# Performance work log

Hardware: AMD Instinct MI355X
Metric: run time of the kernel (lower is better)

Reference implementation:

```python
import jax, jax.numpy as jnp
import numpy as np

B, S, I, H, O = 64, 4096, 256, 256, 128


def setup_inputs() -> dict:
    key = jax.random.key(0)
    ks = jax.random.split(key, 7)
    s_in = 1.0 / np.sqrt(I)
    s_h = 1.0 / np.sqrt(H)
    return {
        "x": jax.random.normal(ks[0], (B, S, I), dtype=jnp.float32),
        "Wax_w": jax.random.uniform(ks[1], (H, I), jnp.float32, -s_in, s_in),
        "Wax_b": jax.random.uniform(ks[2], (H,), jnp.float32, -s_in, s_in),
        "Waa_w": jax.random.uniform(ks[3], (H, H), jnp.float32, -s_h, s_h),
        "Waa_b": jax.random.uniform(ks[4], (H,), jnp.float32, -s_h, s_h),
        "Wya_w": jax.random.uniform(ks[5], (O, H), jnp.float32, -s_h, s_h),
        "Wya_b": jax.random.uniform(ks[6], (O,), jnp.float32, -s_h, s_h),
    }


def reference(x, Wax_w, Wax_b, Waa_w, Waa_b, Wya_w, Wya_b):
    # Precompute input projections for all timesteps in one big GEMM: [B,S,H]
    xp = jnp.einsum("bsi,hi->bsh", x, Wax_w) + Wax_b

    def step(a_prev, xp_t):
        a_next = jnp.tanh(xp_t + a_prev @ Waa_w.T + Waa_b)
        return a_next, None

    a0 = jnp.zeros((x.shape[0], Waa_w.shape[0]), dtype=x.dtype)
    a_last, _ = jax.lax.scan(step, a0, jnp.swapaxes(xp, 0, 1))  # scan over S
    return jax.nn.sigmoid(a_last @ Wya_w.T + Wya_b)
```

## Files before the change

### kernel.cpp

```cpp
#include <hip/hip_runtime.h>
#include <hip/hip_fp16.h>


typedef _Float16 f16x8 __attribute__((ext_vector_type(8)));
typedef _Float16 f16x4 __attribute__((ext_vector_type(4)));
typedef _Float16 f16x2 __attribute__((ext_vector_type(2)));
typedef float    f32x4 __attribute__((ext_vector_type(4)));

#define FDOT2(a, b, c) __builtin_amdgcn_fdot2((a), (b), (c), false)

template <int D>
__device__ __forceinline__ float rorf(float v) {
    return __builtin_bit_cast(float,
        __builtin_amdgcn_update_dpp(0, __builtin_bit_cast(int, v),
                                    0x120 + D, 0xF, 0xF, true));
}
template <int D>
__device__ __forceinline__ float qrot(float v) {
    constexpr int ctrl = D == 1 ? 0x93 : (D == 2 ? 0x4E : 0x39);
    return __builtin_bit_cast(float,
        __builtin_amdgcn_update_dpp(0, __builtin_bit_cast(int, v),
                                    ctrl, 0xF, 0xF, true));
}

__global__ __launch_bounds__(1024) void k_fused(
    const float* __restrict__ x, const float* __restrict__ Ww,
    const float* __restrict__ Wb, const float* __restrict__ Waa,
    const float* __restrict__ Wab, const float* __restrict__ Wya,
    const float* __restrict__ Wyb, float* __restrict__ out,
    _Float16* __restrict__ xp0, _Float16* __restrict__ xp1,
    unsigned short* __restrict__ a_state,
    int c_rnn, int c_xp, int do_rnn, int do_xp, int is_last,
    int T_C, int logT)
{
    __shared__ __align__(16) _Float16 As[128 * 264];
    __shared__ __align__(16) _Float16 aL[2][16][24];
    __shared__ float afin[256];

    const int tid  = threadIdx.x;
    const int lane = tid & 63;

    if (blockIdx.x < 64) {
        if (!do_rnn) return;
        const _Float16* xp = (c_rnn & 1) ? xp1 : xp0;
        const int w     = tid >> 6;
        const int k     = lane & 15;
        const int g     = lane >> 4;
        const int rbase = w * 16 + g * 4;
        const int myrow = rbase + (k & 3);
        const int b     = blockIdx.x;
        const bool wlane = (k & 12) == 0;

        f16x2 wr[4][8];
#pragma unroll
        for (int i = 0; i < 4; ++i) {
            const float4* wp = (const float4*)(Waa + (size_t)(rbase + ((k + i) & 3)) * 256 + k * 16);
#pragma unroll
            for (int q = 0; q < 4; ++q) {
                float4 v = wp[q];
                f16x2 t0; t0[0] = (_Float16)v.x; t0[1] = (_Float16)v.y;
                f16x2 t1; t1[0] = (_Float16)v.z; t1[1] = (_Float16)v.w;
                wr[i][2 * q]     = t0;
                wr[i][2 * q + 1] = t1;
            }
        }
        const float bias = Wab[myrow];

        if (tid < 256) {
            unsigned short v = 0;
            if (c_rnn != 0) v = a_state[b * 256 + tid];
            aL[0][tid >> 4][tid & 15] = __builtin_bit_cast(_Float16, v);
        }
        __syncthreads();

        const _Float16* xph = xp + ((size_t)(b * 256 + myrow)) * T_C;
        f16x8 xq = *(const f16x8*)(xph);
        float bx[8];
#pragma unroll
        for (int j = 0; j < 8; ++j) bx[j] = bias + (float)xq[j];

        const _Float16* rp0 = &aL[0][k][0];
        const _Float16* rp1 = &aL[1][k][0];
        _Float16* wq0 = &aL[1][w][g * 4 + k];
        _Float16* wq1 = &aL[0][w][g * 4 + k];

#define RNN_STEP(J, FIN)                                                     \
    {                                                                        \
        const _Float16* rp = ((J) & 1) ? rp1 : rp0;                          \
        uint4 r0 = *(const uint4*)(rp);                                      \
        uint4 r1 = *(const uint4*)(rp + 8);                                  \
        f16x2 a2[8];                                                         \
        a2[0] = __builtin_bit_cast(f16x2, r0.x);                             \
        a2[1] = __builtin_bit_cast(f16x2, r0.y);                             \
        a2[2] = __builtin_bit_cast(f16x2, r0.z);                             \
        a2[3] = __builtin_bit_cast(f16x2, r0.w);                             \
        a2[4] = __builtin_bit_cast(f16x2, r1.x);                             \
        a2[5] = __builtin_bit_cast(f16x2, r1.y);                             \
        a2[6] = __builtin_bit_cast(f16x2, r1.z);                             \
        a2[7] = __builtin_bit_cast(f16x2, r1.w);                             \
        float s0 = 0.f, s1 = 0.f, s2 = 0.f, s3 = 0.f;                        \
        _Pragma("unroll")                                                    \
        for (int q = 0; q < 8; ++q) {                                        \
            s0 = FDOT2(wr[0][q], a2[q], s0);                                 \
            s1 = FDOT2(wr[1][q], a2[q], s1);                                 \
            s2 = FDOT2(wr[2][q], a2[q], s2);                                 \
            s3 = FDOT2(wr[3][q], a2[q], s3);                                 \
        }                                                                    \
                 \
        float t = s0 + qrot<1>(s1);                                          \
        t += qrot<2>(s2);                                                    \
        t += qrot<3>(s3);                                                    \
        float u   = t + rorf<4>(t);                                          \
        float acc = u + rorf<8>(u);                                          \
        float z  = bx[(J)] + acc;                                            \
        float e2 = __expf(2.f * z);                                          \
        float a  = fmaf(-2.f, __builtin_amdgcn_rcpf(e2 + 1.f), 1.f);         \
        _Float16 ah = (_Float16)a;                                           \
        if (wlane) *(((J) & 1) ? wq1 : wq0) = ah;                            \
        if (FIN) {                                                           \
            afin[myrow] = a;                                                 \
            a_state[b * 256 + myrow] = __builtin_bit_cast(unsigned short, ah);\
        }                                                                    \
        asm volatile("s_waitcnt lgkmcnt(0)" ::: "memory");                   \
        __builtin_amdgcn_s_barrier();                                        \
        asm volatile("" ::: "memory");                                       \
    }

        for (int tb = 0; tb + 8 < T_C; tb += 8) {
            f16x8 xn = *(const f16x8*)(xph + tb + 8);
            RNN_STEP(0, false) RNN_STEP(1, false) RNN_STEP(2, false) RNN_STEP(3, false)
            RNN_STEP(4, false) RNN_STEP(5, false) RNN_STEP(6, false) RNN_STEP(7, false)
#pragma unroll
            for (int j = 0; j < 8; ++j) bx[j] = bias + (float)xn[j];
        }
        RNN_STEP(0, false) RNN_STEP(1, false) RNN_STEP(2, false) RNN_STEP(3, false)
        RNN_STEP(4, false) RNN_STEP(5, false) RNN_STEP(6, false) RNN_STEP(7, true)
#undef RNN_STEP

        if (is_last) {
            const int o  = tid >> 3;
            const int k8 = tid & 7;
            const float4* wp = (const float4*)(Wya + (size_t)o * 256 + k8 * 32);
            const float4* ap = (const float4*)(afin + k8 * 32);
            float s = 0.f;
#pragma unroll
            for (int i = 0; i < 8; ++i) {
                float4 wv4 = wp[i];
                float4 a4  = ap[i];
                s += wv4.x * a4.x + wv4.y * a4.y + wv4.z * a4.z + wv4.w * a4.w;
            }
            s += __shfl_xor(s, 1);
            s += __shfl_xor(s, 2);
            s += __shfl_xor(s, 4);
            if (k8 == 0)
                out[b * 128 + o] = __builtin_amdgcn_rcpf(1.f + __expf(-(s + Wyb[o])));
        }
    } else {
        if (!do_xp) return;
        _Float16* xp = (c_xp & 1) ? xp1 : xp0;
        const int bxp = blockIdx.x - 64;
        const int wv  = tid >> 6;
        const int l15 = lane & 15;
        const int lk  = lane >> 4;
        const int n0  = wv * 16;

        f16x8 bfr[8];
        {
            const float* wrow = Ww + (size_t)(n0 + l15) * 256;
#pragma unroll
            for (int kt = 0; kt < 8; ++kt) {
                const float4* wp = (const float4*)(wrow + kt * 32 + lk * 8);
                float4 v0 = wp[0], v1 = wp[1];
                f16x8 f;
                f[0] = (_Float16)v0.x; f[1] = (_Float16)v0.y;
                f[2] = (_Float16)v0.z; f[3] = (_Float16)v0.w;
                f[4] = (_Float16)v1.x; f[5] = (_Float16)v1.y;
                f[6] = (_Float16)v1.z; f[7] = (_Float16)v1.w;
                bfr[kt] = f;
            }
        }
        const float bias = Wb[n0 + l15];

        {
            const int arow = tid >> 3;
            const int acol = (tid & 7) * 32;
            const int r    = bxp * 128 + arow;
            const int bb   = r >> logT;
            const int tl   = r & (T_C - 1);
            const float4* s4 = (const float4*)(x + ((size_t)(bb * 4096 + c_xp * T_C + tl) << 8) + acol);
            _Float16* d = As + arow * 264 + acol;
#pragma unroll
            for (int q = 0; q < 4; ++q) {
                float4 v0 = s4[2 * q], v1 = s4[2 * q + 1];
                f16x8 p;
                p[0] = (_Float16)v0.x; p[1] = (_Float16)v0.y;
                p[2] = (_Float16)v0.z; p[3] = (_Float16)v0.w;
                p[4] = (_Float16)v1.x; p[5] = (_Float16)v1.y;
                p[6] = (_Float16)v1.z; p[7] = (_Float16)v1.w;
                *(f16x8*)(d + q * 8) = p;
            }
        }
        __syncthreads();

        f32x4 acc[8] = {};
#pragma unroll
        for (int kt = 0; kt < 8; ++kt) {
#pragma unroll
            for (int mt = 0; mt < 8; ++mt) {
                f16x8 af = *(const f16x8*)(As + (mt * 16 + l15) * 264 + kt * 32 + lk * 8);
                acc[mt] = __builtin_amdgcn_mfma_f32_16x16x32_f16(af, bfr[kt], acc[mt], 0, 0, 0);
            }
        }

        const int base = bxp * 128;
#pragma unroll
        for (int mt = 0; mt < 8; ++mt) {
            const int rr  = base + mt * 16 + lk * 4;
            const int bb2 = rr >> logT;
            const int tt  = rr & (T_C - 1);
            f16x4 pk;
#pragma unroll
            for (int r2 = 0; r2 < 4; ++r2) pk[r2] = (_Float16)(acc[mt][r2] + bias);
            *(f16x4*)(xp + ((size_t)(bb2 * 256 + n0 + l15)) * T_C + tt) = pk;
        }
    }
}

extern "C" void kernel_launch(void* const* d_in, const int* in_sizes, int n_in,
                              void* d_out, int out_size, void* d_ws, size_t ws_size,
                              hipStream_t stream)
{
    (void)in_sizes; (void)n_in; (void)out_size;
    const float* x    = (const float*)d_in[0];
    const float* Waxw = (const float*)d_in[1];
    const float* Waxb = (const float*)d_in[2];
    const float* Waaw = (const float*)d_in[3];
    const float* Waab = (const float*)d_in[4];
    const float* Wyaw = (const float*)d_in[5];
    const float* Wyab = (const float*)d_in[6];
    float* out = (float*)d_out;

    int T_C = 1024, logT = 10;
    while (T_C > 128 && (size_t)2 * 64 * T_C * 256 * 2 + 32768 > ws_size) { T_C >>= 1; --logT; }

    _Float16* xp0 = (_Float16*)d_ws;
    _Float16* xp1 = xp0 + (size_t)64 * T_C * 256;
    unsigned short* a_state = (unsigned short*)(xp1 + (size_t)64 * T_C * 256);

    const int nc  = 4096 / T_C;
    const int nxp = 64 * T_C / 128;
    for (int i = 0; i <= nc; ++i) {
        k_fused<<<dim3(64 + nxp), dim3(1024), 0, stream>>>(
            x, Waxw, Waxb, Waaw, Waab, Wyaw, Wyab, out, xp0, xp1, a_state,
            i - 1, i, i >= 1 ? 1 : 0, i < nc ? 1 : 0, i == nc ? 1 : 0,
            T_C, logT);
    }
}
```

Measured before the change: 1.958 ms.

## Process four batch rows per recurrent block to amortize barriers over more work

Each recurrent workgroup now handles four batch elements instead of one, so 16 recurrent blocks run instead of 64. Per step, the shared-memory reads for the next chain are interleaved with the dot-product compute of the current one, and a single barrier covers all four chains. This reuses the register-resident Waa weights across four rows and cuts the number of blocks synchronizing on a per-step barrier. In exchange, each step's critical path grows roughly fourfold within a block and parallelism across CUs drops. A waves-per-EU hint is also added to steer register allocation.

```diff
diff --git a/kernel.cpp b/kernel.cpp
--- a/kernel.cpp
+++ b/kernel.cpp
@@ -23,7 +23,9 @@
                                     ctrl, 0xF, 0xF, true));
 }
 
-__global__ __launch_bounds__(1024) void k_fused(
+__global__ __launch_bounds__(1024)
+__attribute__((amdgpu_waves_per_eu(4, 4)))
+void k_fused(
     const float* __restrict__ x, const float* __restrict__ Ww,
     const float* __restrict__ Wb, const float* __restrict__ Waa,
     const float* __restrict__ Wab, const float* __restrict__ Wya,
@@ -34,13 +36,13 @@
     int T_C, int logT)
 {
     __shared__ __align__(16) _Float16 As[128 * 264];
-    __shared__ __align__(16) _Float16 aL[2][16][24];
-    __shared__ float afin[256];
+    __shared__ __align__(16) _Float16 aL[2][4][16][24];
+    __shared__ float afin[4][256];
 
     const int tid  = threadIdx.x;
     const int lane = tid & 63;
 
-    if (blockIdx.x < 64) {
+    if (blockIdx.x < 16) {
         if (!do_rnn) return;
         const _Float16* xp = (c_rnn & 1) ? xp1 : xp0;
         const int w     = tid >> 6;
@@ -48,7 +50,7 @@
         const int g     = lane >> 4;
         const int rbase = w * 16 + g * 4;
         const int myrow = rbase + (k & 3);
-        const int b     = blockIdx.x;
+        const int bq    = blockIdx.x * 4;
         const bool wlane = (k & 12) == 0;
 
         f16x2 wr[4][8];
@@ -66,99 +68,120 @@
         }
         const float bias = Wab[myrow];
 
-        if (tid < 256) {
+        {
+            const int ch = tid >> 8, r = tid & 255;
             unsigned short v = 0;
-            if (c_rnn != 0) v = a_state[b * 256 + tid];
-            aL[0][tid >> 4][tid & 15] = __builtin_bit_cast(_Float16, v);
+            if (c_rnn != 0) v = a_state[(bq + ch) * 256 + r];
+            aL[0][ch][r >> 4][r & 15] = __builtin_bit_cast(_Float16, v);
         }
         __syncthreads();
 
-        const _Float16* xph = xp + ((size_t)(b * 256 + myrow)) * T_C;
-        f16x8 xq = *(const f16x8*)(xph);
-        float bx[8];
-#pragma unroll
-        for (int j = 0; j < 8; ++j) bx[j] = bias + (float)xq[j];
-
-        const _Float16* rp0 = &aL[0][k][0];
-        const _Float16* rp1 = &aL[1][k][0];
-        _Float16* wq0 = &aL[1][w][g * 4 + k];
-        _Float16* wq1 = &aL[0][w][g * 4 + k];
-
-#define RNN_STEP(J, FIN)                                                     \
-    {                                                                        \
-        const _Float16* rp = ((J) & 1) ? rp1 : rp0;                          \
-        uint4 r0 = *(const uint4*)(rp);                                      \
-        uint4 r1 = *(const uint4*)(rp + 8);                                  \
-        f16x2 a2[8];                                                         \
-        a2[0] = __builtin_bit_cast(f16x2, r0.x);                             \
-        a2[1] = __builtin_bit_cast(f16x2, r0.y);                             \
-        a2[2] = __builtin_bit_cast(f16x2, r0.z);                             \
-        a2[3] = __builtin_bit_cast(f16x2, r0.w);                             \
-        a2[4] = __builtin_bit_cast(f16x2, r1.x);                             \
-        a2[5] = __builtin_bit_cast(f16x2, r1.y);                             \
-        a2[6] = __builtin_bit_cast(f16x2, r1.z);                             \
-        a2[7] = __builtin_bit_cast(f16x2, r1.w);                             \
-        float s0 = 0.f, s1 = 0.f, s2 = 0.f, s3 = 0.f;                        \
-        _Pragma("unroll")                                                    \
-        for (int q = 0; q < 8; ++q) {                                        \
-            s0 = FDOT2(wr[0][q], a2[q], s0);                                 \
-            s1 = FDOT2(wr[1][q], a2[q], s1);                                 \
-            s2 = FDOT2(wr[2][q], a2[q], s2);                                 \
-            s3 = FDOT2(wr[3][q], a2[q], s3);                                 \
-        }                                                                    \
-                 \
-        float t = s0 + qrot<1>(s1);                                          \
-        t += qrot<2>(s2);                                                    \
-        t += qrot<3>(s3);                                                    \
-        float u   = t + rorf<4>(t);                                          \
-        float acc = u + rorf<8>(u);                                          \
-        float z  = bx[(J)] + acc;                                            \
-        float e2 = __expf(2.f * z);                                          \
-        float a  = fmaf(-2.f, __builtin_amdgcn_rcpf(e2 + 1.f), 1.f);         \
-        _Float16 ah = (_Float16)a;                                           \
-        if (wlane) *(((J) & 1) ? wq1 : wq0) = ah;                            \
-        if (FIN) {                                                           \
-            afin[myrow] = a;                                                 \
-            a_state[b * 256 + myrow] = __builtin_bit_cast(unsigned short, ah);\
-        }                                                                    \
-        asm volatile("s_waitcnt lgkmcnt(0)" ::: "memory");                   \
-        __builtin_amdgcn_s_barrier();                                        \
-        asm volatile("" ::: "memory");                                       \
-    }
+        const _Float16* xph[4];
+#pragma unroll
+        for (int ch = 0; ch < 4; ++ch)
+            xph[ch] = xp + ((size_t)((bq + ch) * 256 + myrow)) * T_C;
+        f16x8 xq[4], xn[4];
+#pragma unroll
+        for (int ch = 0; ch < 4; ++ch) xq[ch] = *(const f16x8*)(xph[ch]);
+
+#define DO_READ(CUR, CH, R0, R1)                                             \
+        {                                                                    \
+            const _Float16* rp = &aL[(CUR)][(CH)][k][0];                     \
+            R0 = *(const uint4*)(rp);                                        \
+            R1 = *(const uint4*)(rp + 8);                                    \
+        }
+
+#define DO_COMP(CUR, CH, R0, R1, J, FIN)                                     \
+        {                                                                    \
+            f16x2 a2[8];                                                     \
+            a2[0] = __builtin_bit_cast(f16x2, R0.x);                         \
+            a2[1] = __builtin_bit_cast(f16x2, R0.y);                         \
+            a2[2] = __builtin_bit_cast(f16x2, R0.z);                         \
+            a2[3] = __builtin_bit_cast(f16x2, R0.w);                         \
+            a2[4] = __builtin_bit_cast(f16x2, R1.x);                         \
+            a2[5] = __builtin_bit_cast(f16x2, R1.y);                         \
+            a2[6] = __builtin_bit_cast(f16x2, R1.z);                         \
+            a2[7] = __builtin_bit_cast(f16x2, R1.w);                         \
+            float s0 = 0.f, s1 = 0.f, s2 = 0.f, s3 = 0.f;                    \
+            _Pragma("unroll")                                                \
+            for (int q = 0; q < 8; ++q) {                                    \
+                s0 = FDOT2(wr[0][q], a2[q], s0);                             \
+                s1 = FDOT2(wr[1][q], a2[q], s1);                             \
+                s2 = FDOT2(wr[2][q], a2[q], s2);                             \
+                s3 = FDOT2(wr[3][q], a2[q], s3);                             \
+            }                                                                \
+            float t = s0 + qrot<1>(s1);                                      \
+            t += qrot<2>(s2);                                                \
+            t += qrot<3>(s3);                                                \
+            float u   = t + rorf<4>(t);                                      \
+            float acc = u + rorf<8>(u);                                      \
+            float z  = bias + (float)xq[(CH)][(J)] + acc;                    \
+            float e2 = __expf(2.f * z);                                      \
+            float a  = fmaf(-2.f, __builtin_amdgcn_rcpf(e2 + 1.f), 1.f);     \
+            _Float16 ah = (_Float16)a;                                       \
+            if (wlane) aL[(CUR) ^ 1][(CH)][w][g * 4 + k] = ah;               \
+            if (FIN) {                                                       \
+                afin[(CH)][myrow] = a;                                       \
+                a_state[(bq + (CH)) * 256 + myrow] =                         \
+                    __builtin_bit_cast(unsigned short, ah);                  \
+            }                                                                \
+        }
+
+#define INTERVAL(CUR, J, FIN)                                                \
+        {                                                                    \
+            uint4 ra0, ra1, rb0, rb1, rc0, rc1, rd0, rd1;                    \
+            DO_READ(CUR, 0, ra0, ra1)                                        \
+            DO_READ(CUR, 1, rb0, rb1)                                        \
+            DO_COMP(CUR, 0, ra0, ra1, J, FIN)                                \
+            DO_READ(CUR, 2, rc0, rc1)                                        \
+            DO_COMP(CUR, 1, rb0, rb1, J, FIN)                                \
+            DO_READ(CUR, 3, rd0, rd1)                                        \
+            DO_COMP(CUR, 2, rc0, rc1, J, FIN)                                \
+            DO_COMP(CUR, 3, rd0, rd1, J, FIN)                                \
+            asm volatile("s_waitcnt lgkmcnt(0)" ::: "memory");               \
+            __builtin_amdgcn_s_barrier();                                    \
+            asm volatile("" ::: "memory");                                   \
+        }
 
         for (int tb = 0; tb + 8 < T_C; tb += 8) {
-            f16x8 xn = *(const f16x8*)(xph + tb + 8);
-            RNN_STEP(0, false) RNN_STEP(1, false) RNN_STEP(2, false) RNN_STEP(3, false)
-            RNN_STEP(4, false) RNN_STEP(5, false) RNN_STEP(6, false) RNN_STEP(7, false)
-#pragma unroll
-            for (int j = 0; j < 8; ++j) bx[j] = bias + (float)xn[j];
-        }
-        RNN_STEP(0, false) RNN_STEP(1, false) RNN_STEP(2, false) RNN_STEP(3, false)
-        RNN_STEP(4, false) RNN_STEP(5, false) RNN_STEP(6, false) RNN_STEP(7, true)
-#undef RNN_STEP
+#pragma unroll
+            for (int ch = 0; ch < 4; ++ch)
+                xn[ch] = *(const f16x8*)(xph[ch] + tb + 8);
+            INTERVAL(0, 0, false) INTERVAL(1, 1, false)
+            INTERVAL(0, 2, false) INTERVAL(1, 3, false)
+            INTERVAL(0, 4, false) INTERVAL(1, 5, false)
+            INTERVAL(0, 6, false) INTERVAL(1, 7, false)
+#pragma unroll
+            for (int ch = 0; ch < 4; ++ch) xq[ch] = xn[ch];
+        }
+        INTERVAL(0, 0, false) INTERVAL(1, 1, false)
+        INTERVAL(0, 2, false) INTERVAL(1, 3, false)
+        INTERVAL(0, 4, false) INTERVAL(1, 5, false)
+        INTERVAL(0, 6, false) INTERVAL(1, 7, true)
+#undef INTERVAL
+#undef DO_COMP
+#undef DO_READ
 
         if (is_last) {
-            const int o  = tid >> 3;
-            const int k8 = tid & 7;
-            const float4* wp = (const float4*)(Wya + (size_t)o * 256 + k8 * 32);
-            const float4* ap = (const float4*)(afin + k8 * 32);
-            float s = 0.f;
-#pragma unroll
-            for (int i = 0; i < 8; ++i) {
-                float4 wv4 = wp[i];
-                float4 a4  = ap[i];
-                s += wv4.x * a4.x + wv4.y * a4.y + wv4.z * a4.z + wv4.w * a4.w;
-            }
-            s += __shfl_xor(s, 1);
-            s += __shfl_xor(s, 2);
-            s += __shfl_xor(s, 4);
-            if (k8 == 0)
-                out[b * 128 + o] = __builtin_amdgcn_rcpf(1.f + __expf(-(s + Wyb[o])));
+            const int ch = tid >> 8;
+            if ((tid & 128) == 0) {
+                const int o = tid & 127;
+                const float4* wp = (const float4*)(Wya + (size_t)o * 256);
+                const float4* ap = (const float4*)(&afin[ch][0]);
+                float s = Wyb[o];
+#pragma unroll 8
+                for (int i = 0; i < 64; ++i) {
+                    float4 wv4 = wp[i];
+                    float4 a4  = ap[i];
+                    s += wv4.x * a4.x + wv4.y * a4.y + wv4.z * a4.z + wv4.w * a4.w;
+                }
+                out[(bq + ch) * 128 + o] = __builtin_amdgcn_rcpf(1.f + __expf(-s));
+            }
         }
     } else {
         if (!do_xp) return;
         _Float16* xp = (c_xp & 1) ? xp1 : xp0;
-        const int bxp = blockIdx.x - 64;
+        const int bxp = blockIdx.x - 16;
         const int wv  = tid >> 6;
         const int l15 = lane & 15;
         const int lk  = lane >> 4;
@@ -250,7 +273,7 @@
     const int nc  = 4096 / T_C;
     const int nxp = 64 * T_C / 128;
     for (int i = 0; i <= nc; ++i) {
-        k_fused<<<dim3(64 + nxp), dim3(1024), 0, stream>>>(
+        k_fused<<<dim3(16 + nxp), dim3(1024), 0, stream>>>(
             x, Waxw, Waxb, Waaw, Waab, Wyaw, Wyab, out, xp0, xp1, a_state,
             i - 1, i, i >= 1 ? 1 : 0, i < nc ? 1 : 0, i == nc ? 1 : 0,
             T_C, logT);
```

New measurement: 6.888 ms. 3.52x slower.

## Halve block size to 512 threads, doubling rows per lane in RNN and GEMM

Applied to the files above, without the earlier changes.

Shrinks the block to 512 threads (8 waves). Each RNN lane now handles 8 rows of Waa instead of 4, and the DPP reduction tree is rebuilt for 8 partial sums. The xp GEMM blocks now cover 64 rows by 32 columns per wave, with twice as many blocks. The goal is cheaper per-step barriers in the latency-bound recurrence, since fewer waves synchronise, at the cost of more FDOT2 work and register pressure per lane.

```diff
diff --git a/kernel.cpp b/kernel.cpp
--- a/kernel.cpp
+++ b/kernel.cpp
@@ -15,15 +15,10 @@
         __builtin_amdgcn_update_dpp(0, __builtin_bit_cast(int, v),
                                     0x120 + D, 0xF, 0xF, true));
 }
-template <int D>
-__device__ __forceinline__ float qrot(float v) {
-    constexpr int ctrl = D == 1 ? 0x93 : (D == 2 ? 0x4E : 0x39);
-    return __builtin_bit_cast(float,
-        __builtin_amdgcn_update_dpp(0, __builtin_bit_cast(int, v),
-                                    ctrl, 0xF, 0xF, true));
-}
-
-__global__ __launch_bounds__(1024) void k_fused(
+
+__global__ __launch_bounds__(512)
+__attribute__((amdgpu_waves_per_eu(2, 2)))
+void k_fused(
     const float* __restrict__ x, const float* __restrict__ Ww,
     const float* __restrict__ Wb, const float* __restrict__ Waa,
     const float* __restrict__ Wab, const float* __restrict__ Wya,
@@ -33,7 +28,7 @@
     int c_rnn, int c_xp, int do_rnn, int do_xp, int is_last,
     int T_C, int logT)
 {
-    __shared__ __align__(16) _Float16 As[128 * 264];
+    __shared__ __align__(16) _Float16 As[64 * 264];
     __shared__ __align__(16) _Float16 aL[2][16][24];
     __shared__ float afin[256];
 
@@ -46,15 +41,15 @@
         const int w     = tid >> 6;
         const int k     = lane & 15;
         const int g     = lane >> 4;
-        const int rbase = w * 16 + g * 4;
-        const int myrow = rbase + (k & 3);
+        const int rbase = w * 32 + g * 8;
+        const int myrow = rbase + (k & 7);
         const int b     = blockIdx.x;
-        const bool wlane = (k & 12) == 0;
-
-        f16x2 wr[4][8];
-#pragma unroll
-        for (int i = 0; i < 4; ++i) {
-            const float4* wp = (const float4*)(Waa + (size_t)(rbase + ((k + i) & 3)) * 256 + k * 16);
+        const bool wlane = (k & 8) == 0;
+
+        f16x2 wr[8][8];
+#pragma unroll
+        for (int i = 0; i < 8; ++i) {
+            const float4* wp = (const float4*)(Waa + (size_t)(rbase + ((k + i) & 7)) * 256 + k * 16);
 #pragma unroll
             for (int q = 0; q < 4; ++q) {
                 float4 v = wp[q];
@@ -81,8 +76,8 @@
 
         const _Float16* rp0 = &aL[0][k][0];
         const _Float16* rp1 = &aL[1][k][0];
-        _Float16* wq0 = &aL[1][w][g * 4 + k];
-        _Float16* wq1 = &aL[0][w][g * 4 + k];
+        _Float16* wq0 = &aL[1][myrow >> 4][myrow & 15];
+        _Float16* wq1 = &aL[0][myrow >> 4][myrow & 15];
 
 #define RNN_STEP(J, FIN)                                                     \
     {                                                                        \
@@ -99,19 +94,32 @@
         a2[6] = __builtin_bit_cast(f16x2, r1.z);                             \
         a2[7] = __builtin_bit_cast(f16x2, r1.w);                             \
         float s0 = 0.f, s1 = 0.f, s2 = 0.f, s3 = 0.f;                        \
+        float s4 = 0.f, s5 = 0.f, s6 = 0.f, s7 = 0.f;                        \
         _Pragma("unroll")                                                    \
         for (int q = 0; q < 8; ++q) {                                        \
             s0 = FDOT2(wr[0][q], a2[q], s0);                                 \
             s1 = FDOT2(wr[1][q], a2[q], s1);                                 \
             s2 = FDOT2(wr[2][q], a2[q], s2);                                 \
             s3 = FDOT2(wr[3][q], a2[q], s3);                                 \
+            s4 = FDOT2(wr[4][q], a2[q], s4);                                 \
+            s5 = FDOT2(wr[5][q], a2[q], s5);                                 \
+            s6 = FDOT2(wr[6][q], a2[q], s6);                                 \
+            s7 = FDOT2(wr[7][q], a2[q], s7);                                 \
         }                                                                    \
-                 \
-        float t = s0 + qrot<1>(s1);                                          \
-        t += qrot<2>(s2);                                                    \
-        t += qrot<3>(s3);                                                    \
-        float u   = t + rorf<4>(t);                                          \
-        float acc = u + rorf<8>(u);                                          \
+                                                  \
+        float p0 = s0 + rorf<8>(s0);                                         \
+        float p1 = s1 + rorf<8>(s1);                                         \
+        float p2 = s2 + rorf<8>(s2);                                         \
+        float p3 = s3 + rorf<8>(s3);                                         \
+        float p4 = s4 + rorf<8>(s4);                                         \
+        float p5 = s5 + rorf<8>(s5);                                         \
+        float p6 = s6 + rorf<8>(s6);                                         \
+        float p7 = s7 + rorf<8>(s7);                                         \
+        float q0 = p0 + rorf<4>(p4);                                         \
+        float q1 = p1 + rorf<4>(p5);                                         \
+        float q2 = p2 + rorf<4>(p6);                                         \
+        float q3 = p3 + rorf<4>(p7);                                         \
+        float acc = (q0 + rorf<1>(q1)) + (rorf<2>(q2) + rorf<3>(q3));        \
         float z  = bx[(J)] + acc;                                            \
         float e2 = __expf(2.f * z);                                          \
         float a  = fmaf(-2.f, __builtin_amdgcn_rcpf(e2 + 1.f), 1.f);         \
@@ -138,21 +146,20 @@
 #undef RNN_STEP
 
         if (is_last) {
-            const int o  = tid >> 3;
-            const int k8 = tid & 7;
-            const float4* wp = (const float4*)(Wya + (size_t)o * 256 + k8 * 32);
-            const float4* ap = (const float4*)(afin + k8 * 32);
+            const int o  = tid >> 2;
+            const int k4 = tid & 3;
+            const float4* wp = (const float4*)(Wya + (size_t)o * 256 + k4 * 64);
+            const float4* ap = (const float4*)(afin + k4 * 64);
             float s = 0.f;
 #pragma unroll
-            for (int i = 0; i < 8; ++i) {
+            for (int i = 0; i < 16; ++i) {
                 float4 wv4 = wp[i];
                 float4 a4  = ap[i];
                 s += wv4.x * a4.x + wv4.y * a4.y + wv4.z * a4.z + wv4.w * a4.w;
             }
             s += __shfl_xor(s, 1);
             s += __shfl_xor(s, 2);
-            s += __shfl_xor(s, 4);
-            if (k8 == 0)
+            if (k4 == 0)
                 out[b * 128 + o] = __builtin_amdgcn_rcpf(1.f + __expf(-(s + Wyb[o])));
         }
     } else {
@@ -162,11 +169,12 @@
         const int wv  = tid >> 6;
         const int l15 = lane & 15;
         const int lk  = lane >> 4;
-        const int n0  = wv * 16;
-
-        f16x8 bfr[8];
-        {
-            const float* wrow = Ww + (size_t)(n0 + l15) * 256;
+        const int n0  = wv * 32;
+
+        f16x8 bfr[2][8];
+#pragma unroll
+        for (int nt = 0; nt < 2; ++nt) {
+            const float* wrow = Ww + (size_t)(n0 + nt * 16 + l15) * 256;
 #pragma unroll
             for (int kt = 0; kt < 8; ++kt) {
                 const float4* wp = (const float4*)(wrow + kt * 32 + lk * 8);
@@ -176,15 +184,16 @@
                 f[2] = (_Float16)v0.z; f[3] = (_Float16)v0.w;
                 f[4] = (_Float16)v1.x; f[5] = (_Float16)v1.y;
                 f[6] = (_Float16)v1.z; f[7] = (_Float16)v1.w;
-                bfr[kt] = f;
-            }
-        }
-        const float bias = Wb[n0 + l15];
+                bfr[nt][kt] = f;
+            }
+        }
+        const float bias0 = Wb[n0 + l15];
+        const float bias1 = Wb[n0 + 16 + l15];
 
         {
             const int arow = tid >> 3;
             const int acol = (tid & 7) * 32;
-            const int r    = bxp * 128 + arow;
+            const int r    = bxp * 64 + arow;
             const int bb   = r >> logT;
             const int tl   = r & (T_C - 1);
             const float4* s4 = (const float4*)(x + ((size_t)(bb * 4096 + c_xp * T_C + tl) << 8) + acol);
@@ -202,26 +211,32 @@
         }
         __syncthreads();
 
-        f32x4 acc[8] = {};
+        f32x4 acc[4][2] = {};
 #pragma unroll
         for (int kt = 0; kt < 8; ++kt) {
 #pragma unroll
-            for (int mt = 0; mt < 8; ++mt) {
+            for (int mt = 0; mt < 4; ++mt) {
                 f16x8 af = *(const f16x8*)(As + (mt * 16 + l15) * 264 + kt * 32 + lk * 8);
-                acc[mt] = __builtin_amdgcn_mfma_f32_16x16x32_f16(af, bfr[kt], acc[mt], 0, 0, 0);
-            }
-        }
-
-        const int base = bxp * 128;
-#pragma unroll
-        for (int mt = 0; mt < 8; ++mt) {
+                acc[mt][0] = __builtin_amdgcn_mfma_f32_16x16x32_f16(af, bfr[0][kt], acc[mt][0], 0, 0, 0);
+                acc[mt][1] = __builtin_amdgcn_mfma_f32_16x16x32_f16(af, bfr[1][kt], acc[mt][1], 0, 0, 0);
+            }
+        }
+
+        const int base = bxp * 64;
+#pragma unroll
+        for (int mt = 0; mt < 4; ++mt) {
             const int rr  = base + mt * 16 + lk * 4;
             const int bb2 = rr >> logT;
             const int tt  = rr & (T_C - 1);
-            f16x4 pk;
-#pragma unroll
-            for (int r2 = 0; r2 < 4; ++r2) pk[r2] = (_Float16)(acc[mt][r2] + bias);
-            *(f16x4*)(xp + ((size_t)(bb2 * 256 + n0 + l15)) * T_C + tt) = pk;
+#pragma unroll
+            for (int nt = 0; nt < 2; ++nt) {
+                const int   h    = n0 + nt * 16 + l15;
+                const float bias = (nt == 0) ? bias0 : bias1;
+                f16x4 pk;
+#pragma unroll
+                for (int r2 = 0; r2 < 4; ++r2) pk[r2] = (_Float16)(acc[mt][nt][r2] + bias);
+                *(f16x4*)(xp + ((size_t)(bb2 * 256 + h)) * T_C + tt) = pk;
+            }
         }
     }
 }
@@ -248,9 +263,9 @@
     unsigned short* a_state = (unsigned short*)(xp1 + (size_t)64 * T_C * 256);
 
     const int nc  = 4096 / T_C;
-    const int nxp = 64 * T_C / 128;
+    const int nxp = T_C;
     for (int i = 0; i <= nc; ++i) {
-        k_fused<<<dim3(64 + nxp), dim3(1024), 0, stream>>>(
+        k_fused<<<dim3(64 + nxp), dim3(512), 0, stream>>>(
             x, Waxw, Waxb, Waaw, Waab, Wyaw, Wyab, out, xp0, xp1, a_state,
             i - 1, i, i >= 1 ? 1 : 0, i < nc ? 1 : 0, i == nc ? 1 : 0,
             T_C, logT);
```

Measured after the change: 1.913 ms, median of 2. 1.02x faster.
